# Optimization experiments

Measured on AMD Instinct MI355X. Metric: run time of the kernel, lower is better.

The kernel has to match this reference:

```python
import jax, jax.numpy as jnp
import numpy as np

N = 100000   # nodes
E = 1200000  # edges
IN = 128     # input feature dim
H = 64       # hidden_channels
OUT = 112    # output classes
L = 7        # num_layers
MSG_EPS = 1e-7


def _ln(x, g, b):
    mu = x.mean(-1, keepdims=True)
    v = ((x - mu) ** 2).mean(-1, keepdims=True)
    return (x - mu) / jnp.sqrt(v + 1e-5) * g + b


def _genconv(x, src, dst, t, scale, W1, b1, g1, bb1, W2, b2):
    # message: relu(x_j) + eps  (no edge attrs)
    m = jax.nn.relu(x[src]) + MSG_EPS                     # [E, H]
    z = t * m
    # numerically stable per-dst softmax over incoming edges (per channel)
    zmax = jax.lax.stop_gradient(jax.ops.segment_max(z, dst, num_segments=N))
    e = jnp.exp(z - zmax[dst])
    denom = jax.ops.segment_sum(e, dst, num_segments=N)
    agg = jax.ops.segment_sum(m * e, dst, num_segments=N) / jnp.where(denom > 0, denom, 1.0)
    # MsgNorm: x + scale * ||x|| * normalize(agg)
    msg = agg / jnp.maximum(jnp.linalg.norm(agg, axis=-1, keepdims=True), 1e-12)
    h = x + scale * msg * jnp.linalg.norm(x, axis=-1, keepdims=True)
    # GENConv MLP: Linear(H,2H) -> LayerNorm -> ReLU -> Linear(2H,H)
    u = jax.nn.relu(_ln(h @ W1 + b1, g1, bb1))
    return u @ W2 + b2


def setup_inputs() -> dict:
    key = jax.random.key(0)
    ks = jax.random.split(key, 6)
    s = 0.02
    return dict(
        x=jax.random.normal(ks[0], (N, IN), jnp.float32),
        edge_index=jax.random.randint(ks[1], (2, E), 0, N, dtype=jnp.int32),
        enc_W=jax.random.normal(ks[2], (IN, H), jnp.float32) * s,
        enc_b=jnp.zeros((H,), jnp.float32),
        t=jnp.ones((L,), jnp.float32),
        msg_scale=jnp.ones((L,), jnp.float32),
        W1=jax.random.normal(ks[3], (L, H, 2 * H), jnp.float32) * s,
        b1=jnp.zeros((L, 2 * H), jnp.float32),
        ln1_g=jnp.ones((L, 2 * H), jnp.float32),
        ln1_b=jnp.zeros((L, 2 * H), jnp.float32),
        W2=jax.random.normal(ks[4], (L, 2 * H, H), jnp.float32) * s,
        b2=jnp.zeros((L, H), jnp.float32),
        nrm_g=jnp.ones((L, H), jnp.float32),
        nrm_b=jnp.zeros((L, H), jnp.float32),
        lin_W=jax.random.normal(ks[5], (H, OUT), jnp.float32) * s,
        lin_b=jnp.zeros((OUT,), jnp.float32),
    )


def reference(x, edge_index, enc_W, enc_b, t, msg_scale, W1, b1, ln1_g, ln1_b,
              W2, b2, nrm_g, nrm_b, lin_W, lin_b):
    src, dst = edge_index[0], edge_index[1]
    h = x @ enc_W + enc_b
    # first layer: conv only (DeeperGCN forward applies layers[0].conv directly)
    h = _genconv(h, src, dst, t[0], msg_scale[0], W1[0], b1[0], ln1_g[0], ln1_b[0], W2[0], b2[0])
    # remaining layers: res+ block  x + conv(dropout(relu(norm(x))))  (dropout=identity at eval)
    for i in range(1, L):
        r = jax.nn.relu(_ln(h, nrm_g[i], nrm_b[i]))
        h = h + _genconv(r, src, dst, t[i], msg_scale[i], W1[i], b1[i], ln1_g[i], ln1_b[i], W2[i], b2[i])
    h = jax.nn.relu(_ln(h, nrm_g[0], nrm_b[0]))
    return h @ lin_W + lin_b
```

## Files before the change

### kernel.cpp

```cpp
#include <hip/hip_runtime.h>

#define N_NODES 100000
#define N_EDGES 1200000
#define DIM_IN 128
#define DIM_H 64
#define DIM_H2 128
#define DIM_OUT 112
#define N_LAYERS 7

#define W1P_SZ 4608
#define W2P_SZ 4352
#define WEP_SZ 4352
#define WFP_SZ 4032

typedef __attribute__((ext_vector_type(8))) short bf16x8;
typedef __attribute__((ext_vector_type(4))) float f32x4;
typedef __attribute__((ext_vector_type(2))) float f32x2;

__device__ __forceinline__ unsigned bf16rne(float f) {
  unsigned u = __float_as_uint(f);
  return (u + 0x7fffu + ((u >> 16) & 1u)) >> 16;
}
__device__ __forceinline__ unsigned pack2bf(float lo, float hi) {
  return bf16rne(lo) | (bf16rne(hi) << 16);
}
__device__ __forceinline__ float bflo(unsigned p) { return __uint_as_float(p << 16); }
__device__ __forceinline__ float bfhi(unsigned p) { return __uint_as_float(p & 0xffff0000u); }
__device__ __forceinline__ float exp2r(float x) { return __builtin_amdgcn_exp2f(x); }


__global__ void k_zero_i(int* __restrict__ p, int n) {
  int i = blockIdx.x * 256 + threadIdx.x;
  if (i < n) p[i] = 0;
}

__global__ void k_hist(const int* __restrict__ dst, int* __restrict__ counts,
                       int* __restrict__ rank) {
  int e = blockIdx.x * 256 + threadIdx.x;
  if (e < N_EDGES) rank[e] = atomicAdd(&counts[dst[e]], 1);
}

__global__ void k_scan1(const int* __restrict__ counts, int* __restrict__ bsums) {
  __shared__ int sd[256];
  int t = threadIdx.x;
  int i = blockIdx.x * 256 + t;
  sd[t] = (i < N_NODES) ? counts[i] : 0;
  __syncthreads();
  for (int s = 128; s > 0; s >>= 1) {
    if (t < s) sd[t] += sd[t + s];
    __syncthreads();
  }
  if (t == 0) bsums[blockIdx.x] = sd[0];
}

__global__ void k_scan2(int* __restrict__ bsums, int nb) {
  __shared__ int sd[512];
  int t = threadIdx.x;
  int v = (t < nb) ? bsums[t] : 0;
  sd[t] = v;
  __syncthreads();
  for (int o = 1; o < 512; o <<= 1) {
    int add = (t >= o) ? sd[t - o] : 0;
    __syncthreads();
    sd[t] += add;
    __syncthreads();
  }
  if (t < nb) bsums[t] = sd[t] - v;
}

__global__ void k_scan3(const int* __restrict__ counts, const int* __restrict__ bsums,
                        int* __restrict__ offs) {
  __shared__ int sd[256];
  int t = threadIdx.x;
  int i = blockIdx.x * 256 + t;
  int v = (i < N_NODES) ? counts[i] : 0;
  sd[t] = v;
  __syncthreads();
  for (int o = 1; o < 256; o <<= 1) {
    int add = (t >= o) ? sd[t - o] : 0;
    __syncthreads();
    sd[t] += add;
    __syncthreads();
  }
  int excl = sd[t] - v + bsums[blockIdx.x];
  if (i < N_NODES) offs[i] = excl;
  if (i == N_NODES - 1) offs[N_NODES] = excl + v;
}

__global__ void k_scatter(const int* __restrict__ src, const int* __restrict__ dst,
                          const int* __restrict__ rank, const int* __restrict__ offs,
                          int* __restrict__ ssrc) {
  int e = blockIdx.x * 256 + threadIdx.x;
  if (e < N_EDGES) {
    int p = offs[dst[e]] + rank[e];
    ssrc[p] = src[e];
  }
}


__global__ void k_prepack(const float* __restrict__ W1, const float* __restrict__ W2,
                          unsigned* __restrict__ W1p, unsigned* __restrict__ W2p) {
  int L = blockIdx.y;
  const float* w1 = W1 + (size_t)L * DIM_H * DIM_H2;
  const float* w2 = W2 + (size_t)L * DIM_H2 * DIM_H;
  unsigned* o1 = W1p + (size_t)L * W1P_SZ;
  unsigned* o2 = W2p + (size_t)L * W2P_SZ;
  for (int i = blockIdx.x * 256 + threadIdx.x; i < W1P_SZ; i += gridDim.x * 256) {
    int n = i / 36, kp = i - n * 36;
    o1[i] = (kp < 32) ? pack2bf(w1[(size_t)(2 * kp) * DIM_H2 + n],
                                w1[(size_t)(2 * kp + 1) * DIM_H2 + n]) : 0u;
  }
  for (int i = blockIdx.x * 256 + threadIdx.x; i < W2P_SZ; i += gridDim.x * 256) {
    int n = i / 68, kp = i - n * 68;
    o2[i] = (kp < 64) ? pack2bf(w2[(size_t)(2 * kp) * DIM_H + n],
                                w2[(size_t)(2 * kp + 1) * DIM_H + n]) : 0u;
  }
}

__global__ void k_prepack_enc(const float* __restrict__ W, unsigned* __restrict__ Wp) {
  for (int i = blockIdx.x * 256 + threadIdx.x; i < WEP_SZ; i += gridDim.x * 256) {
    int n = i / 68, kp = i - n * 68;
    Wp[i] = (kp < 64) ? pack2bf(W[(size_t)(2 * kp) * DIM_H + n],
                                W[(size_t)(2 * kp + 1) * DIM_H + n]) : 0u;
  }
}

__global__ void k_prepack_fin(const float* __restrict__ W, unsigned* __restrict__ Wp) {
  for (int i = blockIdx.x * 256 + threadIdx.x; i < WFP_SZ; i += gridDim.x * 256) {
    int n = i / 36, kp = i - n * 36;
    Wp[i] = (kp < 32) ? pack2bf(W[(size_t)(2 * kp) * DIM_OUT + n],
                                W[(size_t)(2 * kp + 1) * DIM_OUT + n]) : 0u;
  }
}


__global__ __launch_bounds__(256, 2) void k_encoder(const float* __restrict__ x,
                                                    const unsigned* __restrict__ Wp,
                                                    const float* __restrict__ bias,
                                                    unsigned short* __restrict__ hBf) {
  __shared__ __attribute__((aligned(16))) unsigned sW[WEP_SZ];
  __shared__ __attribute__((aligned(16))) unsigned sxp[32 * 68];
  int t = threadIdx.x;
  int node0 = blockIdx.x * 32;
  int w = t >> 6, lane = t & 63;
  int fr = lane & 15, fq = lane >> 4;
  const uint4* wv4 = (const uint4*)Wp;
  for (int i = t; i < WEP_SZ / 4; i += 256) *(uint4*)&sW[i * 4] = wv4[i];
  for (int i = t; i < 2048; i += 256) {
    int row = i >> 6, kp = i & 63;
    float2 xv = *(const float2*)&x[(size_t)(node0 + row) * DIM_IN + 2 * kp];
    sxp[row * 68 + kp] = pack2bf(xv.x, xv.y);
  }
  __syncthreads();
  f32x4 acc0 = {0.f, 0.f, 0.f, 0.f}, acc1 = acc0;
#pragma unroll
  for (int s = 0; s < 4; s++) {
    int kp0 = s * 16 + fq * 4;
    bf16x8 a0 = *(const bf16x8*)&sxp[fr * 68 + kp0];
    bf16x8 a1 = *(const bf16x8*)&sxp[(16 + fr) * 68 + kp0];
    bf16x8 wf = *(const bf16x8*)&sW[(w * 16 + fr) * 68 + kp0];
    acc0 = __builtin_amdgcn_mfma_f32_16x16x32_bf16(a0, wf, acc0, 0, 0, 0);
    acc1 = __builtin_amdgcn_mfma_f32_16x16x32_bf16(a1, wf, acc1, 0, 0, 0);
  }
  float bv = bias[w * 16 + fr];
#pragma unroll
  for (int r = 0; r < 4; r++) {
    hBf[(size_t)(node0 + fq * 4 + r) * DIM_H + w * 16 + fr] =
        (unsigned short)bf16rne(acc0[r] + bv);
    hBf[(size_t)(node0 + 16 + fq * 4 + r) * DIM_H + w * 16 + fr] =
        (unsigned short)bf16rne(acc1[r] + bv);
  }
}


template <int RELU>
__global__ __launch_bounds__(256) void k_edge(const unsigned* __restrict__ xin32,
                                              const int* __restrict__ ssrc,
                                              const int* __restrict__ offs,
                                              const float* __restrict__ t_arr,
                                              const float* __restrict__ sc_arr, int layer,
                                              unsigned* __restrict__ hmid32) {
  int t = threadIdx.x;
  int wave = t >> 6, lane = t & 63;
  int half = lane >> 5, cl = lane & 31;
  int v = blockIdx.x * 8 + wave * 2 + half;
  float c2 = t_arr[layer] * 1.4426950408889634f;
  f32x2 c2v = {c2, c2};
  float sc = sc_arr[layer];
  int beg = offs[v], end = offs[v + 1];
  unsigned cl4 = cl << 2;
  const char* xbase = (const char*)xin32;
  unsigned xp = *(const unsigned*)(xbase + (((unsigned)v << 7) + cl4));
  float xv0 = bflo(xp), xv1 = bfhi(xp);
  f32x2 Dv0 = {0.f, 0.f}, Dv1 = Dv0, Dv2 = Dv0, Dv3 = Dv0;
  f32x2 Sv0 = Dv0, Sv1 = Dv0, Sv2 = Dv0, Sv3 = Dv0;
  int e = beg;
#define UNPK(u, m)                                     \
  f32x2 m;                                             \
  m.x = RELU ? fmaxf(bflo(u), 0.f) : bflo(u);          \
  m.y = RELU ? fmaxf(bfhi(u), 0.f) : bfhi(u);
#define EXPV(m, ev)                                    \
  f32x2 ev;                                            \
  {                                                    \
    f32x2 z_ = c2v * m;                                \
    ev.x = exp2r(z_.x);                                \
    ev.y = exp2r(z_.y);                                \
  }
  for (; e + 7 < end; e += 8) {
    unsigned o0 = ((unsigned)ssrc[e] << 7) + cl4;
    unsigned o1 = ((unsigned)ssrc[e + 1] << 7) + cl4;
    unsigned o2 = ((unsigned)ssrc[e + 2] << 7) + cl4;
    unsigned o3 = ((unsigned)ssrc[e + 3] << 7) + cl4;
    unsigned o4 = ((unsigned)ssrc[e + 4] << 7) + cl4;
    unsigned o5 = ((unsigned)ssrc[e + 5] << 7) + cl4;
    unsigned o6 = ((unsigned)ssrc[e + 6] << 7) + cl4;
    unsigned o7 = ((unsigned)ssrc[e + 7] << 7) + cl4;
    unsigned u0 = *(const unsigned*)(xbase + o0);
    unsigned u1 = *(const unsigned*)(xbase + o1);
    unsigned u2 = *(const unsigned*)(xbase + o2);
    unsigned u3 = *(const unsigned*)(xbase + o3);
    unsigned u4 = *(const unsigned*)(xbase + o4);
    unsigned u5 = *(const unsigned*)(xbase + o5);
    unsigned u6 = *(const unsigned*)(xbase + o6);
    unsigned u7 = *(const unsigned*)(xbase + o7);
    UNPK(u0, m0) UNPK(u1, m1) UNPK(u2, m2) UNPK(u3, m3)
    UNPK(u4, m4) UNPK(u5, m5) UNPK(u6, m6) UNPK(u7, m7)
    EXPV(m0, e0) EXPV(m1, e1) EXPV(m2, e2) EXPV(m3, e3)
    EXPV(m4, e4) EXPV(m5, e5) EXPV(m6, e6) EXPV(m7, e7)
    Dv0 += e0; Sv0 += m0 * e0;
    Dv1 += e1; Sv1 += m1 * e1;
    Dv2 += e2; Sv2 += m2 * e2;
    Dv3 += e3; Sv3 += m3 * e3;
    Dv0 += e4; Sv0 += m4 * e4;
    Dv1 += e5; Sv1 += m5 * e5;
    Dv2 += e6; Sv2 += m6 * e6;
    Dv3 += e7; Sv3 += m7 * e7;
  }
  if (e + 3 < end) {
    unsigned o0 = ((unsigned)ssrc[e] << 7) + cl4;
    unsigned o1 = ((unsigned)ssrc[e + 1] << 7) + cl4;
    unsigned o2 = ((unsigned)ssrc[e + 2] << 7) + cl4;
    unsigned o3 = ((unsigned)ssrc[e + 3] << 7) + cl4;
    unsigned u0 = *(const unsigned*)(xbase + o0);
    unsigned u1 = *(const unsigned*)(xbase + o1);
    unsigned u2 = *(const unsigned*)(xbase + o2);
    unsigned u3 = *(const unsigned*)(xbase + o3);
    UNPK(u0, m0) UNPK(u1, m1) UNPK(u2, m2) UNPK(u3, m3)
    EXPV(m0, e0) EXPV(m1, e1) EXPV(m2, e2) EXPV(m3, e3)
    Dv0 += e0; Sv0 += m0 * e0;
    Dv1 += e1; Sv1 += m1 * e1;
    Dv2 += e2; Sv2 += m2 * e2;
    Dv3 += e3; Sv3 += m3 * e3;
    e += 4;
  }
  for (; e < end; ++e) {
    unsigned o0 = ((unsigned)ssrc[e] << 7) + cl4;
    unsigned u0 = *(const unsigned*)(xbase + o0);
    UNPK(u0, m0)
    EXPV(m0, e0)
    Dv0 += e0; Sv0 += m0 * e0;
  }
#undef UNPK
#undef EXPV
  f32x2 Dt = (Dv0 + Dv1) + (Dv2 + Dv3);
  f32x2 St = (Sv0 + Sv1) + (Sv2 + Sv3);
  int has = (end > beg);
  float agg0 = has ? (St.x / Dt.x + 1e-7f) : 0.f;
  float agg1 = has ? (St.y / Dt.y + 1e-7f) : 0.f;
  float na = agg0 * agg0 + agg1 * agg1;
  float nx = xv0 * xv0 + xv1 * xv1;
#pragma unroll
  for (int m = 1; m < 32; m <<= 1) {
    na += __shfl_xor(na, m, 64);
    nx += __shfl_xor(nx, m, 64);
  }
  float inv = sc * sqrtf(nx) / fmaxf(sqrtf(na), 1e-12f);
  float r0 = xv0 + inv * agg0;
  float r1 = xv1 + inv * agg1;
  hmid32[(size_t)v * 32 + cl] = pack2bf(r0, r1);
}


__global__ __launch_bounds__(256, 2) void k_mlp(const unsigned* __restrict__ xin32,
                                                float* __restrict__ h,
                                                unsigned short* __restrict__ rnext,
                                                const unsigned* __restrict__ W1p,
                                                const float* __restrict__ b1,
                                                const float* __restrict__ g1,
                                                const float* __restrict__ bb1,
                                                const unsigned* __restrict__ W2p,
                                                const float* __restrict__ b2,
                                                const float* __restrict__ gn,
                                                const float* __restrict__ bn, int residual) {
  __shared__ unsigned short scr[4][16][136];
  int t = threadIdx.x;
  int w = t >> 6, lane = t & 63;
  int wid = blockIdx.x * 4 + w;
  if (wid >= N_NODES / 16) return;
  int node0 = wid * 16;
  int fr = lane & 15, fq = lane >> 4;

  bf16x8 xa0 = *(const bf16x8*)&xin32[(size_t)(node0 + fr) * 32 + fq * 4];
  bf16x8 xa1 = *(const bf16x8*)&xin32[(size_t)(node0 + fr) * 32 + 16 + fq * 4];
  f32x4 c1[8];
#pragma unroll
  for (int nt = 0; nt < 8; nt++) {
    f32x4 a = {0.f, 0.f, 0.f, 0.f};
    bf16x8 w0 = *(const bf16x8*)&W1p[(size_t)(nt * 16 + fr) * 36 + fq * 4];
    bf16x8 w1 = *(const bf16x8*)&W1p[(size_t)(nt * 16 + fr) * 36 + 16 + fq * 4];
    a = __builtin_amdgcn_mfma_f32_16x16x32_bf16(xa0, w0, a, 0, 0, 0);
    a = __builtin_amdgcn_mfma_f32_16x16x32_bf16(xa1, w1, a, 0, 0, 0);
    c1[nt] = a;
  }
  float b1v[8], g1v[8], bb1v[8];
#pragma unroll
  for (int nt = 0; nt < 8; nt++) {
    b1v[nt] = b1[nt * 16 + fr];
    g1v[nt] = g1[nt * 16 + fr];
    bb1v[nt] = bb1[nt * 16 + fr];
  }
#pragma unroll
  for (int r = 0; r < 4; r++) {
    float s1 = 0.f, s2 = 0.f;
#pragma unroll
    for (int nt = 0; nt < 8; nt++) {
      float u = c1[nt][r] + b1v[nt];
      s1 += u;
      s2 += u * u;
    }
#pragma unroll
    for (int m = 1; m < 16; m <<= 1) {
      s1 += __shfl_xor(s1, m, 64);
      s2 += __shfl_xor(s2, m, 64);
    }
    float mu = s1 * (1.f / 128.f);
    float var = s2 * (1.f / 128.f) - mu * mu;
    float rs = rsqrtf(var + 1e-5f);
    int row = fq * 4 + r;
#pragma unroll
    for (int nt = 0; nt < 8; nt++) {
      float u = c1[nt][r] + b1v[nt];
      u = fmaxf((u - mu) * rs * g1v[nt] + bb1v[nt], 0.f);
      scr[w][row][nt * 16 + fr] = (unsigned short)bf16rne(u);
    }
  }
  bf16x8 ua[4];
#pragma unroll
  for (int s = 0; s < 4; s++) ua[s] = *(const bf16x8*)&scr[w][fr][s * 32 + fq * 8];
  f32x4 c2[4];
#pragma unroll
  for (int nt = 0; nt < 4; nt++) {
    f32x4 a = {0.f, 0.f, 0.f, 0.f};
#pragma unroll
    for (int s = 0; s < 4; s++) {
      bf16x8 wf = *(const bf16x8*)&W2p[(size_t)(nt * 16 + fr) * 68 + s * 16 + fq * 4];
      a = __builtin_amdgcn_mfma_f32_16x16x32_bf16(ua[s], wf, a, 0, 0, 0);
    }
    c2[nt] = a;
  }
  float b2v[4], gv[4], bv[4];
#pragma unroll
  for (int nt = 0; nt < 4; nt++) {
    b2v[nt] = b2[nt * 16 + fr];
    gv[nt] = gn[nt * 16 + fr];
    bv[nt] = bn[nt * 16 + fr];
  }
#pragma unroll
  for (int r = 0; r < 4; r++) {
    int row = fq * 4 + r;
    size_t base = (size_t)(node0 + row) * DIM_H;
    float o0, o1, o2, o3, s1, s2;
    o0 = c2[0][r] + b2v[0];
    o1 = c2[1][r] + b2v[1];
    o2 = c2[2][r] + b2v[2];
    o3 = c2[3][r] + b2v[3];
    if (residual) {
      o0 += h[base + 0 * 16 + fr];
      o1 += h[base + 1 * 16 + fr];
      o2 += h[base + 2 * 16 + fr];
      o3 += h[base + 3 * 16 + fr];
    }
    s1 = (o0 + o1) + (o2 + o3);
    s2 = (o0 * o0 + o1 * o1) + (o2 * o2 + o3 * o3);
#pragma unroll
    for (int m = 1; m < 16; m <<= 1) {
      s1 += __shfl_xor(s1, m, 64);
      s2 += __shfl_xor(s2, m, 64);
    }
    float mu = s1 * (1.f / 64.f);
    float var = s2 * (1.f / 64.f) - mu * mu;
    float rs = rsqrtf(var + 1e-5f);
    h[base + 0 * 16 + fr] = o0;
    h[base + 1 * 16 + fr] = o1;
    h[base + 2 * 16 + fr] = o2;
    h[base + 3 * 16 + fr] = o3;
    rnext[base + 0 * 16 + fr] = (unsigned short)bf16rne(fmaxf((o0 - mu) * rs * gv[0] + bv[0], 0.f));
    rnext[base + 1 * 16 + fr] = (unsigned short)bf16rne(fmaxf((o1 - mu) * rs * gv[1] + bv[1], 0.f));
    rnext[base + 2 * 16 + fr] = (unsigned short)bf16rne(fmaxf((o2 - mu) * rs * gv[2] + bv[2], 0.f));
    rnext[base + 3 * 16 + fr] = (unsigned short)bf16rne(fmaxf((o3 - mu) * rs * gv[3] + bv[3], 0.f));
  }
}


__global__ __launch_bounds__(256, 2) void k_final(const unsigned* __restrict__ rB32,
                                                  const unsigned* __restrict__ Wp,
                                                  const float* __restrict__ bias,
                                                  float* __restrict__ out) {
  int t = threadIdx.x;
  int w = t >> 6, lane = t & 63;
  int wid = blockIdx.x * 4 + w;
  if (wid >= N_NODES / 16) return;
  int node0 = wid * 16;
  int fr = lane & 15, fq = lane >> 4;
  bf16x8 xa0 = *(const bf16x8*)&rB32[(size_t)(node0 + fr) * 32 + fq * 4];
  bf16x8 xa1 = *(const bf16x8*)&rB32[(size_t)(node0 + fr) * 32 + 16 + fq * 4];
#pragma unroll
  for (int nt = 0; nt < 7; nt++) {
    f32x4 a = {0.f, 0.f, 0.f, 0.f};
    bf16x8 w0 = *(const bf16x8*)&Wp[(size_t)(nt * 16 + fr) * 36 + fq * 4];
    bf16x8 w1 = *(const bf16x8*)&Wp[(size_t)(nt * 16 + fr) * 36 + 16 + fq * 4];
    a = __builtin_amdgcn_mfma_f32_16x16x32_bf16(xa0, w0, a, 0, 0, 0);
    a = __builtin_amdgcn_mfma_f32_16x16x32_bf16(xa1, w1, a, 0, 0, 0);
    float bv = bias[nt * 16 + fr];
#pragma unroll
    for (int r = 0; r < 4; r++)
      out[(size_t)(node0 + fq * 4 + r) * DIM_OUT + nt * 16 + fr] = a[r] + bv;
  }
}


extern "C" void kernel_launch(void* const* d_in, const int* in_sizes, int n_in,
                              void* d_out, int out_size, void* d_ws, size_t ws_size,
                              hipStream_t stream) {
  const float* x = (const float*)d_in[0];
  const int* ei = (const int*)d_in[1];
  const float* encW = (const float*)d_in[2];
  const float* encb = (const float*)d_in[3];
  const float* t_arr = (const float*)d_in[4];
  const float* sc_arr = (const float*)d_in[5];
  const float* W1 = (const float*)d_in[6];
  const float* b1 = (const float*)d_in[7];
  const float* g1 = (const float*)d_in[8];
  const float* bb1 = (const float*)d_in[9];
  const float* W2 = (const float*)d_in[10];
  const float* b2 = (const float*)d_in[11];
  const float* ng = (const float*)d_in[12];
  const float* nbias = (const float*)d_in[13];
  const float* linW = (const float*)d_in[14];
  const float* linb = (const float*)d_in[15];

  float* hA = (float*)d_ws;
  unsigned short* mCbf = (unsigned short*)(hA + (size_t)N_NODES * DIM_H);
  unsigned short* rBf = mCbf + (size_t)N_NODES * DIM_H;
  unsigned short* hBf = rBf + (size_t)N_NODES * DIM_H;
  int* ssrc = (int*)(hBf + (size_t)N_NODES * DIM_H);
  int* rank = ssrc + N_EDGES;
  int* offs = rank + N_EDGES;
  int* counts = offs + (N_NODES + 1);
  int* bsums = counts + N_NODES;
  unsigned* W1p = (unsigned*)(((uintptr_t)(bsums + 512) + 15) & ~(uintptr_t)15);
  unsigned* W2p = W1p + (size_t)N_LAYERS * W1P_SZ;
  unsigned* Wep = W2p + (size_t)N_LAYERS * W2P_SZ;
  unsigned* Wfp = Wep + WEP_SZ;

  const int* srcI = ei;
  const int* dstI = ei + N_EDGES;

  const int nbScan = (N_NODES + 255) / 256;
  const int nbEdge = (N_EDGES + 255) / 256;
  const int nbWave = (N_NODES / 16 + 3) / 4;

  k_zero_i<<<nbScan, 256, 0, stream>>>(counts, N_NODES);
  k_hist<<<nbEdge, 256, 0, stream>>>(dstI, counts, rank);
  k_prepack<<<dim3(3, N_LAYERS), 256, 0, stream>>>(W1, W2, W1p, W2p);
  k_prepack_enc<<<3, 256, 0, stream>>>(encW, Wep);
  k_prepack_fin<<<3, 256, 0, stream>>>(linW, Wfp);
  k_scan1<<<nbScan, 256, 0, stream>>>(counts, bsums);
  k_scan2<<<1, 512, 0, stream>>>(bsums, nbScan);
  k_scan3<<<nbScan, 256, 0, stream>>>(counts, bsums, offs);
  k_scatter<<<nbEdge, 256, 0, stream>>>(srcI, dstI, rank, offs, ssrc);

  k_encoder<<<N_NODES / 32, 256, 0, stream>>>(x, Wep, encb, hBf);

  for (int i = 0; i < N_LAYERS; i++) {
    int nx = (i + 1 < N_LAYERS) ? (i + 1) : 0;
    const unsigned* gin32 = (const unsigned*)((i == 0) ? hBf : rBf);
    if (i == 0)
      k_edge<1><<<N_NODES / 8, 256, 0, stream>>>(gin32, ssrc, offs, t_arr, sc_arr, i,
                                                 (unsigned*)mCbf);
    else
      k_edge<0><<<N_NODES / 8, 256, 0, stream>>>(gin32, ssrc, offs, t_arr, sc_arr, i,
                                                 (unsigned*)mCbf);
    k_mlp<<<nbWave, 256, 0, stream>>>(
        (const unsigned*)mCbf, hA, rBf, W1p + (size_t)i * W1P_SZ, b1 + i * DIM_H2,
        g1 + i * DIM_H2, bb1 + i * DIM_H2, W2p + (size_t)i * W2P_SZ, b2 + i * DIM_H,
        ng + nx * DIM_H, nbias + nx * DIM_H, (i > 0) ? 1 : 0);
  }

  k_final<<<nbWave, 256, 0, stream>>>((const unsigned*)rBf, Wfp, linb, (float*)d_out);
}
```

Before: 554.2 us.

## Sort nodes by in-degree for edge kernel and pad histogram counters

Adds a counting sort of nodes by in-degree (histogram, scan, scatter into a permutation), and the edge aggregation kernel now processes nodes in that order, so the two half-waves paired in a wave have similar edge counts and less divergent tail work. Histogram counters are also spaced 64 bytes apart to reduce atomic contention on shared cache lines. This adds three small preprocessing kernels, a larger zeroed counter array, and scattered output writes from the edge kernel, since permuted nodes no longer write contiguously.

```diff
diff --git a/kernel.cpp b/kernel.cpp
--- a/kernel.cpp
+++ b/kernel.cpp
@@ -34,17 +34,17 @@
   if (i < n) p[i] = 0;
 }
 
-__global__ void k_hist(const int* __restrict__ dst, int* __restrict__ counts,
+__global__ void k_hist(const int* __restrict__ dst, int* __restrict__ counts16,
                        int* __restrict__ rank) {
   int e = blockIdx.x * 256 + threadIdx.x;
-  if (e < N_EDGES) rank[e] = atomicAdd(&counts[dst[e]], 1);
-}
-
-__global__ void k_scan1(const int* __restrict__ counts, int* __restrict__ bsums) {
+  if (e < N_EDGES) rank[e] = atomicAdd(&counts16[(size_t)dst[e] * 16], 1);
+}
+
+__global__ void k_scan1(const int* __restrict__ counts16, int* __restrict__ bsums) {
   __shared__ int sd[256];
   int t = threadIdx.x;
   int i = blockIdx.x * 256 + t;
-  sd[t] = (i < N_NODES) ? counts[i] : 0;
+  sd[t] = (i < N_NODES) ? counts16[(size_t)i * 16] : 0;
   __syncthreads();
   for (int s = 128; s > 0; s >>= 1) {
     if (t < s) sd[t] += sd[t + s];
@@ -68,12 +68,12 @@
   if (t < nb) bsums[t] = sd[t] - v;
 }
 
-__global__ void k_scan3(const int* __restrict__ counts, const int* __restrict__ bsums,
+__global__ void k_scan3(const int* __restrict__ counts16, const int* __restrict__ bsums,
                         int* __restrict__ offs) {
   __shared__ int sd[256];
   int t = threadIdx.x;
   int i = blockIdx.x * 256 + t;
-  int v = (i < N_NODES) ? counts[i] : 0;
+  int v = (i < N_NODES) ? counts16[(size_t)i * 16] : 0;
   sd[t] = v;
   __syncthreads();
   for (int o = 1; o < 256; o <<= 1) {
@@ -95,6 +95,55 @@
     int p = offs[dst[e]] + rank[e];
     ssrc[p] = src[e];
   }
+}
+
+
+__global__ void k_dhist(const int* __restrict__ offs, int* __restrict__ dbuck) {
+  __shared__ int lh[64];
+  int t = threadIdx.x;
+  int i = blockIdx.x * 256 + t;
+  if (t < 64) lh[t] = 0;
+  __syncthreads();
+  if (i < N_NODES) {
+    int deg = offs[i + 1] - offs[i];
+    atomicAdd(&lh[min(deg, 63)], 1);
+  }
+  __syncthreads();
+  if (t < 64 && lh[t]) atomicAdd(&dbuck[t], lh[t]);
+}
+
+__global__ void k_dscan(const int* __restrict__ dbuck, int* __restrict__ dcursor) {
+  __shared__ int sd[64];
+  int t = threadIdx.x;
+  int v = dbuck[t];
+  sd[t] = v;
+  __syncthreads();
+  for (int o = 1; o < 64; o <<= 1) {
+    int add = (t >= o) ? sd[t - o] : 0;
+    __syncthreads();
+    sd[t] += add;
+    __syncthreads();
+  }
+  dcursor[t] = sd[t] - v;
+}
+
+__global__ void k_dscatter(const int* __restrict__ offs, int* __restrict__ dcursor,
+                           int* __restrict__ perm) {
+  __shared__ int lh[64], lbase[64];
+  int t = threadIdx.x;
+  int i = blockIdx.x * 256 + t;
+  if (t < 64) lh[t] = 0;
+  __syncthreads();
+  int b = 0, lr = 0;
+  if (i < N_NODES) {
+    int deg = offs[i + 1] - offs[i];
+    b = min(deg, 63);
+    lr = atomicAdd(&lh[b], 1);
+  }
+  __syncthreads();
+  if (t < 64) lbase[t] = lh[t] ? atomicAdd(&dcursor[t], lh[t]) : 0;
+  __syncthreads();
+  if (i < N_NODES) perm[lbase[b] + lr] = i;
 }
 
 
@@ -177,13 +226,15 @@
 __global__ __launch_bounds__(256) void k_edge(const unsigned* __restrict__ xin32,
                                               const int* __restrict__ ssrc,
                                               const int* __restrict__ offs,
+                                              const int* __restrict__ perm,
                                               const float* __restrict__ t_arr,
                                               const float* __restrict__ sc_arr, int layer,
                                               unsigned* __restrict__ hmid32) {
   int t = threadIdx.x;
   int wave = t >> 6, lane = t & 63;
   int half = lane >> 5, cl = lane & 31;
-  int v = blockIdx.x * 8 + wave * 2 + half;
+  int gid = blockIdx.x * 8 + wave * 2 + half;
+  int v = perm[gid];
   float c2 = t_arr[layer] * 1.4426950408889634f;
   f32x2 c2v = {c2, c2};
   float sc = sc_arr[layer];
@@ -456,9 +507,12 @@
   int* ssrc = (int*)(hBf + (size_t)N_NODES * DIM_H);
   int* rank = ssrc + N_EDGES;
   int* offs = rank + N_EDGES;
-  int* counts = offs + (N_NODES + 1);
-  int* bsums = counts + N_NODES;
-  unsigned* W1p = (unsigned*)(((uintptr_t)(bsums + 512) + 15) & ~(uintptr_t)15);
+  int* perm = offs + (N_NODES + 1);
+  int* counts16 = perm + N_NODES;
+  int* bsums = counts16 + (size_t)16 * N_NODES;
+  int* dbuck = bsums + 512;
+  int* dcursor = dbuck + 64;
+  unsigned* W1p = (unsigned*)(((uintptr_t)(dcursor + 64) + 15) & ~(uintptr_t)15);
   unsigned* W2p = W1p + (size_t)N_LAYERS * W1P_SZ;
   unsigned* Wep = W2p + (size_t)N_LAYERS * W2P_SZ;
   unsigned* Wfp = Wep + WEP_SZ;
@@ -470,15 +524,19 @@
   const int nbEdge = (N_EDGES + 255) / 256;
   const int nbWave = (N_NODES / 16 + 3) / 4;
 
-  k_zero_i<<<nbScan, 256, 0, stream>>>(counts, N_NODES);
-  k_hist<<<nbEdge, 256, 0, stream>>>(dstI, counts, rank);
+  k_zero_i<<<(16 * N_NODES + 255) / 256, 256, 0, stream>>>(counts16, 16 * N_NODES);
+  k_zero_i<<<1, 256, 0, stream>>>(dbuck, 64);
+  k_hist<<<nbEdge, 256, 0, stream>>>(dstI, counts16, rank);
   k_prepack<<<dim3(3, N_LAYERS), 256, 0, stream>>>(W1, W2, W1p, W2p);
   k_prepack_enc<<<3, 256, 0, stream>>>(encW, Wep);
   k_prepack_fin<<<3, 256, 0, stream>>>(linW, Wfp);
-  k_scan1<<<nbScan, 256, 0, stream>>>(counts, bsums);
+  k_scan1<<<nbScan, 256, 0, stream>>>(counts16, bsums);
   k_scan2<<<1, 512, 0, stream>>>(bsums, nbScan);
-  k_scan3<<<nbScan, 256, 0, stream>>>(counts, bsums, offs);
+  k_scan3<<<nbScan, 256, 0, stream>>>(counts16, bsums, offs);
   k_scatter<<<nbEdge, 256, 0, stream>>>(srcI, dstI, rank, offs, ssrc);
+  k_dhist<<<nbScan, 256, 0, stream>>>(offs, dbuck);
+  k_dscan<<<1, 64, 0, stream>>>(dbuck, dcursor);
+  k_dscatter<<<nbScan, 256, 0, stream>>>(offs, dcursor, perm);
 
   k_encoder<<<N_NODES / 32, 256, 0, stream>>>(x, Wep, encb, hBf);
 
@@ -486,11 +544,11 @@
     int nx = (i + 1 < N_LAYERS) ? (i + 1) : 0;
     const unsigned* gin32 = (const unsigned*)((i == 0) ? hBf : rBf);
     if (i == 0)
-      k_edge<1><<<N_NODES / 8, 256, 0, stream>>>(gin32, ssrc, offs, t_arr, sc_arr, i,
-                                                 (unsigned*)mCbf);
+      k_edge<1><<<N_NODES / 8, 256, 0, stream>>>(gin32, ssrc, offs, perm, t_arr, sc_arr,
+                                                 i, (unsigned*)mCbf);
     else
-      k_edge<0><<<N_NODES / 8, 256, 0, stream>>>(gin32, ssrc, offs, t_arr, sc_arr, i,
-                                                 (unsigned*)mCbf);
+      k_edge<0><<<N_NODES / 8, 256, 0, stream>>>(gin32, ssrc, offs, perm, t_arr, sc_arr,
+                                                 i, (unsigned*)mCbf);
     k_mlp<<<nbWave, 256, 0, stream>>>(
         (const unsigned*)mCbf, hA, rBf, W1p + (size_t)i * W1P_SZ, b1 + i * DIM_H2,
         g1 + i * DIM_H2, bb1 + i * DIM_H2, W2p + (size_t)i * W2P_SZ, b2 + i * DIM_H,
```

Result: no change. 544.4 us (-1.8%).
